# Kernel tuning notes

Measured on AMD Instinct MI355X. Metric: run time of the kernel, lower is better.

The kernel has to match this reference:

```python
import jax, jax.numpy as jnp
import numpy as np

N, E, B, O = 100000, 1600000, 256, 32
D, H, OD = 128, 128, 32  # node_features, hidden_dim, order_encoding_dim
L = 3  # num_layers


def setup_inputs() -> dict:
    key = jax.random.key(0)
    ks = jax.random.split(key, 32)
    g = lambda k, s, fan: jax.random.normal(k, s, jnp.float32) * (1.0 / np.sqrt(fan))
    inp = {
        'x': jax.random.normal(ks[0], (N, D), jnp.float32),
        'edge_index': jax.random.randint(ks[1], (2, E), 0, N),
        'orders': jax.random.normal(ks[2], (B, O, OD), jnp.float32),
        'batch': jnp.sort(jax.random.randint(ks[3], (N,), 0, B)),
        # GIN layers (input_dim == hidden_dim so all 3 layers stack): MLP = Lin(H,H)->ReLU->Lin(H,H), then BatchNorm1d
        'gW1': g(ks[4], (L, H, H), H), 'gb1': jnp.zeros((L, H)),
        'gW2': g(ks[5], (L, H, H), H), 'gb2': jnp.zeros((L, H)),
        'gamma': jnp.ones((L, H)), 'beta': jnp.zeros((L, H)),
        # order encoder: Lin(OD,H)->ReLU->Lin(H,H)
        'oW1': g(ks[6], (OD, H), OD), 'ob1': jnp.zeros((H,)),
        'oW2': g(ks[7], (H, H), H), 'ob2': jnp.zeros((H,)),
        # score head: Lin(4H,H)->ReLU->Lin(H,H//2)->ReLU->Lin(H//2,1)
        'sW1': g(ks[8], (4 * H, H), 4 * H), 'sb1': jnp.zeros((H,)),
        'sW2': g(ks[9], (H, H // 2), H), 'sb2': jnp.zeros((H // 2,)),
        'sW3': g(ks[10], (H // 2, 1), H // 2), 'sb3': jnp.zeros((1,)),
    }
    return inp


def reference(x, edge_index, orders, batch, gW1, gb1, gW2, gb2, gamma, beta,
              oW1, ob1, oW2, ob2, sW1, sb1, sW2, sb2, sW3, sb3):
    n = x.shape[0]
    src, dst = edge_index[0], edge_index[1]
    h = x
    nl = gW1.shape[0]
    for i in range(nl):  # fixed small layer count
        agg = jax.ops.segment_sum(h[src], dst, num_segments=n)  # sum aggregation
        z = agg + h  # (1 + eps) * x with eps = 0 (GINConv default)
        z = jnp.maximum(z @ gW1[i] + gb1[i], 0) @ gW2[i] + gb2[i]
        mu = z.mean(0)
        var = z.var(0)  # biased var, as torch BN uses for normalization
        z = (z - mu) * jax.lax.rsqrt(var + 1e-5) * gamma[i] + beta[i]
        h = jnp.maximum(z, 0) if i < nl - 1 else z  # dropout inactive (eval)
    b = orders.shape[0]
    cnt = jax.ops.segment_sum(jnp.ones((n,), h.dtype), batch, num_segments=b)
    ssum = jax.ops.segment_sum(h, batch, num_segments=b)
    smean = ssum / jnp.maximum(cnt, 1)[:, None]
    smax = jax.ops.segment_max(h, batch, num_segments=b)
    smax = jnp.where(jnp.isfinite(smax), smax, 0)
    graph = jnp.concatenate([smean, smax, ssum], axis=-1)  # [B, 3H]
    # batched over num_orders (equivalent to the python per-order loop)
    oe = jnp.maximum(orders @ oW1 + ob1, 0) @ oW2 + ob2  # [B, O, H]
    comb = jnp.concatenate(
        [jnp.broadcast_to(graph[:, None, :], (b, orders.shape[1], graph.shape[-1])), oe], axis=-1)
    s = jnp.maximum(comb @ sW1 + sb1, 0)
    s = jnp.maximum(s @ sW2 + sb2, 0)
    s = (s @ sW3 + sb3)[..., 0]  # [B, O]
    return s
```

## Files before the change

kernel.cpp:

```cpp
#include <hip/hip_runtime.h>

static constexpr int NN = 100000;
static constexpr int NE = 1600000;
static constexpr int NB = 256;
static constexpr int NO = 32;
static constexpr int HD = 128;
static constexpr long NH = (long)NN * HD;

static constexpr int BSHIFT = 9;
static constexpr int BSIZE = 1 << BSHIFT;
static constexpr int NBUCK = 256;
static constexpr int BCAP = 10240;
static constexpr int CHUNK = 16384;
static constexpr int NCHUNK = (NE + CHUNK - 1) / CHUNK;
static constexpr int POOL_ROWS = 64;
static constexpr int POOL_GRID = (NN + POOL_ROWS - 1) / POOL_ROWS;
static constexpr int NSUB = 64;
static constexpr int GATHER_GRID = NN / 4;

typedef _Float16 f16x8 __attribute__((ext_vector_type(8)));
typedef _Float16 f16x4 __attribute__((ext_vector_type(4)));
typedef _Float16 f16x2 __attribute__((ext_vector_type(2)));
typedef float f32x4 __attribute__((ext_vector_type(4)));

__device__ __forceinline__ unsigned int encf(float f) {
  unsigned int u = __float_as_uint(f);
  return (u & 0x80000000u) ? ~u : (u | 0x80000000u);
}
__device__ __forceinline__ float decf(unsigned int e) {
  return (e & 0x80000000u) ? __uint_as_float(e & 0x7fffffffu) : __uint_as_float(~e);
}

__global__ void bucket_scatter(const int* __restrict__ ei, int* __restrict__ cursor,
                               unsigned int* __restrict__ binned) {
  __shared__ int cnt[NBUCK];
  __shared__ int runbase[NBUCK];
  const int t = threadIdx.x;
  cnt[t] = 0;
  __syncthreads();
  long start = (long)blockIdx.x * CHUNK;
  long end = min((long)NE, start + CHUNK);
  for (long e = start + t; e < end; e += 256)
    atomicAdd(&cnt[ei[NE + e] >> BSHIFT], 1);
  __syncthreads();
  int c = cnt[t];
  runbase[t] = c ? atomicAdd(&cursor[t], c) : 0;
  cnt[t] = 0;
  __syncthreads();
  for (long e = start + t; e < end; e += 256) {
    int d = ei[NE + e], s = ei[e];
    int b = d >> BSHIFT;
    int pos = b * BCAP + runbase[b] + atomicAdd(&cnt[b], 1);
    binned[pos] = ((unsigned int)s << BSHIFT) | (unsigned int)(d & (BSIZE - 1));
  }
}

__global__ void bucket_csr(const unsigned int* __restrict__ binned,
                           const int* __restrict__ cursor,
                           int* __restrict__ rowStart, int* __restrict__ rowEnd,
                           int* __restrict__ col) {
  __shared__ int cnt[BSIZE];
  __shared__ int excl[BSIZE];
  __shared__ int cur[BSIZE];
  __shared__ int part[256];
  const int b = blockIdx.x;
  const int t = threadIdx.x;
  const int lo = b * BCAP;
  const int hi = lo + cursor[b];
  cnt[t] = 0; cnt[t + 256] = 0;
  __syncthreads();
  for (int i = lo + t; i < hi; i += 256)
    atomicAdd(&cnt[binned[i] & (BSIZE - 1)], 1);
  __syncthreads();
  int a0 = cnt[2 * t], a1 = cnt[2 * t + 1];
  int s = a0 + a1;
  part[t] = s;
  __syncthreads();
  for (int off = 1; off < 256; off <<= 1) {
    int u = (t >= off) ? part[t - off] : 0;
    __syncthreads();
    part[t] += u;
    __syncthreads();
  }
  int ebase = part[t] - s;
  excl[2 * t] = ebase;
  excl[2 * t + 1] = ebase + a0;
  __syncthreads();
  const int node0 = b * BSIZE;
  for (int i = t; i < BSIZE; i += 256) {
    int node = node0 + i;
    if (node < NN) {
      rowStart[node] = lo + excl[i];
      rowEnd[node]   = lo + excl[i] + cnt[i];
    }
    cur[i] = lo + excl[i];
  }
  __syncthreads();
  for (int i = lo + t; i < hi; i += 256) {
    unsigned int v = binned[i];
    int pos = atomicAdd(&cur[v & (BSIZE - 1)], 1);
    col[pos] = (int)(v >> BSHIFT);
  }
}

__global__ void f32to16_kernel(const float* __restrict__ in, _Float16* __restrict__ out) {
  long i = (long)(blockIdx.x * 256 + threadIdx.x) * 8;
  if (i >= NH) return;
  float4 a = *reinterpret_cast<const float4*>(in + i);
  float4 b = *reinterpret_cast<const float4*>(in + i + 4);
  f16x8 v;
  v[0] = (_Float16)a.x; v[1] = (_Float16)a.y; v[2] = (_Float16)a.z; v[3] = (_Float16)a.w;
  v[4] = (_Float16)b.x; v[5] = (_Float16)b.y; v[6] = (_Float16)b.z; v[7] = (_Float16)b.w;
  *reinterpret_cast<f16x8*>(out + i) = v;
}

__global__ void pack_w_kernel(const float* __restrict__ gW1, const float* __restrict__ gW2,
                              _Float16* __restrict__ Wp) {
  int tid = blockIdx.x * blockDim.x + threadIdx.x;
  if (tid >= 12288) return;
  int lane = tid & 63;
  int s = (tid >> 6) & 3;
  int t = (tid >> 8) & 7;
  int which = (tid >> 11) & 1;
  int layer = tid >> 12;
  const float* W = (which ? gW2 : gW1) + (long)layer * 128 * 128;
  _Float16* dst = Wp + (long)tid * 8;
  int kbase = s * 32 + ((lane >> 4) << 3);
  int n = t * 16 + (lane & 15);
#pragma unroll
  for (int j = 0; j < 8; ++j) dst[j] = (_Float16)W[(kbase + j) * 128 + n];
}

__global__ void pack_head_kernel(const float* __restrict__ oW1, const float* __restrict__ oW2,
                                 const float* __restrict__ sW1, const float* __restrict__ sW2,
                                 _Float16* __restrict__ dst) {
  int tid = blockIdx.x * blockDim.x + threadIdx.x;
  if (tid >= 5632) return;
  const float* W; int K, N, rowOff;
  int base = tid;
  if (tid < 512)       { W = oW1; K = 32;  N = 128; rowOff = 0;   }
  else if (tid < 2560) { W = oW2; K = 128; N = 128; rowOff = 0;   base = tid - 512; }
  else if (tid < 4608) { W = sW1; K = 128; N = 128; rowOff = 384; base = tid - 2560; }
  else                 { W = sW2; K = 128; N = 64;  rowOff = 0;   base = tid - 4608; }
  int lane = base & 63;
  int fs = base >> 6;
  int NS = K >> 5;
  int s = fs % NS;
  int tt = fs / NS;
  int k = s * 32 + ((lane >> 4) << 3);
  int n = tt * 16 + (lane & 15);
  _Float16* d = dst + (long)tid * 8;
#pragma unroll
  for (int j = 0; j < 8; ++j) d[j] = (_Float16)W[(long)(rowOff + k + j) * N + n];
}

__global__ void gather_kernel(const _Float16* __restrict__ hin, const int* __restrict__ rowStart,
                              const int* __restrict__ rowEnd, const int* __restrict__ col,
                              _Float16* __restrict__ z) {
  const int node = (blockIdx.x * blockDim.x + threadIdx.x) >> 6;
  if (node >= NN) return;
  const int c2 = (threadIdx.x & 63) * 2;
  auto ldh = [&](int n) -> float2 {
    f16x2 h = *reinterpret_cast<const f16x2*>(hin + (long)n * HD + c2);
    return make_float2((float)h[0], (float)h[1]);
  };
  const int lo = rowStart[node];
  const int hi = rowEnd[node];
  float2 acc = ldh(node);
  int j = lo;
  for (; j + 4 <= hi; j += 4) {
    int s0 = col[j], s1 = col[j + 1], s2 = col[j + 2], s3 = col[j + 3];
    float2 v0 = ldh(s0), v1 = ldh(s1), v2 = ldh(s2), v3 = ldh(s3);
    acc.x += (v0.x + v1.x) + (v2.x + v3.x);
    acc.y += (v0.y + v1.y) + (v2.y + v3.y);
  }
  if (j < hi) {
    int last = hi - 1;
    int s0 = col[j];
    int s1 = col[min(j + 1, last)];
    int s2 = col[min(j + 2, last)];
    int s3 = col[min(j + 3, last)];
    float m1 = (j + 1 < hi) ? 1.f : 0.f;
    float m2 = (j + 2 < hi) ? 1.f : 0.f;
    float m3 = (j + 3 < hi) ? 1.f : 0.f;
    float2 v0 = ldh(s0), v1 = ldh(s1), v2 = ldh(s2), v3 = ldh(s3);
    acc.x += v0.x + m1 * v1.x + m2 * v2.x + m3 * v3.x;
    acc.y += v0.y + m1 * v1.y + m2 * v2.y + m3 * v3.y;
  }
  f16x2 o;
  o[0] = (_Float16)acc.x;
  o[1] = (_Float16)acc.y;
  *reinterpret_cast<f16x2*>(z + (long)node * HD + c2) = o;
}

__global__ void __launch_bounds__(256)
fused_layer(const _Float16* __restrict__ Z, const _Float16* __restrict__ Wp,
            const float* __restrict__ b1, const float* __restrict__ b2,
            _Float16* __restrict__ Z2, float* __restrict__ accum2) {
  __shared__ _Float16 Abuf[64 * 136];
  __shared__ float red[256];
  const int t = threadIdx.x;
  const int row0 = blockIdx.x * 64;
  const int lane = t & 63;
  const int w = t >> 6;
  const int l15 = lane & 15;
  const int kgrp = lane >> 4;

  for (int idx = t; idx < 64 * 16; idx += 256) {
    int r = idx >> 4;
    int c8 = (idx & 15) * 8;
    int row = row0 + r;
    f16x8 v = {};
    if (row < NN) v = *reinterpret_cast<const f16x8*>(Z + (long)row * HD + c8);
    *reinterpret_cast<f16x8*>(&Abuf[r * 136 + c8]) = v;
  }
  red[t] = 0.f;
  __syncthreads();

  f32x4 acc[8];
  {
    f16x8 af[4];
#pragma unroll
    for (int s = 0; s < 4; ++s)
      af[s] = *reinterpret_cast<const f16x8*>(&Abuf[(w * 16 + l15) * 136 + s * 32 + kgrp * 8]);
    const _Float16* W1p = Wp;
#pragma unroll
    for (int tt = 0; tt < 8; ++tt) {
      float bb = b1[tt * 16 + l15];
      acc[tt] = (f32x4){bb, bb, bb, bb};
#pragma unroll
      for (int s = 0; s < 4; ++s) {
        f16x8 bf = *reinterpret_cast<const f16x8*>(W1p + ((tt * 4 + s) * 64 + lane) * 8);
        acc[tt] = __builtin_amdgcn_mfma_f32_16x16x32_f16(af[s], bf, acc[tt], 0, 0, 0);
      }
    }
  }
#pragma unroll
  for (int tt = 0; tt < 8; ++tt) {
#pragma unroll
    for (int j = 0; j < 4; ++j) {
      float v = fmaxf(acc[tt][j], 0.f);
      Abuf[(w * 16 + kgrp * 4 + j) * 136 + tt * 16 + l15] = (_Float16)v;
    }
  }
  {
    f16x8 af[4];
#pragma unroll
    for (int s = 0; s < 4; ++s)
      af[s] = *reinterpret_cast<const f16x8*>(&Abuf[(w * 16 + l15) * 136 + s * 32 + kgrp * 8]);
    const _Float16* W2p = Wp + 16384;
#pragma unroll
    for (int tt = 0; tt < 8; ++tt) {
      float bb = b2[tt * 16 + l15];
      acc[tt] = (f32x4){bb, bb, bb, bb};
#pragma unroll
      for (int s = 0; s < 4; ++s) {
        f16x8 bf = *reinterpret_cast<const f16x8*>(W2p + ((tt * 4 + s) * 64 + lane) * 8);
        acc[tt] = __builtin_amdgcn_mfma_f32_16x16x32_f16(af[s], bf, acc[tt], 0, 0, 0);
      }
    }
  }
#pragma unroll
  for (int tt = 0; tt < 8; ++tt) {
    int c = tt * 16 + l15;
    float s = 0.f, q = 0.f;
#pragma unroll
    for (int j = 0; j < 4; ++j) {
      int r = row0 + w * 16 + kgrp * 4 + j;
      if (r < NN) {
        float v = acc[tt][j];
        Z2[(long)r * HD + c] = (_Float16)v;
        s += v; q += v * v;
      }
    }
    atomicAdd(&red[c], s);
    atomicAdd(&red[128 + c], q);
  }
  __syncthreads();
  atomicAdd(&accum2[(blockIdx.x & (NSUB - 1)) * 256 + t], red[t]);
}

__global__ void bn_reduce(const float* __restrict__ accum2, const float* __restrict__ gamma,
                          const float* __restrict__ beta, float* __restrict__ scsh) {
  const int c = threadIdx.x;
  float s = 0.f;
  for (int i = 0; i < NSUB; ++i) s += accum2[i * 256 + c];
  __shared__ float red[256];
  red[c] = s;
  __syncthreads();
  if (c < 128) {
    const float n = (float)NN;
    float mu = red[c] / n;
    float var = red[128 + c] / n - mu * mu;
    float sc = rsqrtf(var + 1e-5f) * gamma[c];
    scsh[c] = sc;
    scsh[128 + c] = beta[c] - mu * sc;
  }
}

__global__ void bn_apply(const _Float16* __restrict__ z2, const float* __restrict__ scsh,
                         _Float16* __restrict__ hn) {
  long idx = (long)blockIdx.x * 256 + threadIdx.x;
  if (idx >= (long)NN * 16) return;
  int c8 = ((int)idx & 15) * 8;
  float4 sc0 = *reinterpret_cast<const float4*>(scsh + c8);
  float4 sc1 = *reinterpret_cast<const float4*>(scsh + c8 + 4);
  float4 sh0 = *reinterpret_cast<const float4*>(scsh + 128 + c8);
  float4 sh1 = *reinterpret_cast<const float4*>(scsh + 128 + c8 + 4);
  f16x8 v = *reinterpret_cast<const f16x8*>(z2 + idx * 8);
  f16x8 o;
  o[0] = (_Float16)fmaxf(fmaf((float)v[0], sc0.x, sh0.x), 0.f);
  o[1] = (_Float16)fmaxf(fmaf((float)v[1], sc0.y, sh0.y), 0.f);
  o[2] = (_Float16)fmaxf(fmaf((float)v[2], sc0.z, sh0.z), 0.f);
  o[3] = (_Float16)fmaxf(fmaf((float)v[3], sc0.w, sh0.w), 0.f);
  o[4] = (_Float16)fmaxf(fmaf((float)v[4], sc1.x, sh1.x), 0.f);
  o[5] = (_Float16)fmaxf(fmaf((float)v[5], sc1.y, sh1.y), 0.f);
  o[6] = (_Float16)fmaxf(fmaf((float)v[6], sc1.z, sh1.z), 0.f);
  o[7] = (_Float16)fmaxf(fmaf((float)v[7], sc1.w, sh1.w), 0.f);
  *reinterpret_cast<f16x8*>(hn + idx * 8) = o;
}

__global__ void pool_init(float* __restrict__ ssum, unsigned int* __restrict__ smaxU) {
  int i = blockIdx.x * 256 + threadIdx.x;
  ssum[i] = 0.f;
  smaxU[i] = 0x007FFFFFu;
}

__global__ void pool_partial(const _Float16* __restrict__ z2, const float* __restrict__ scsh,
                             const int* __restrict__ batch,
                             float* __restrict__ ssum, unsigned int* __restrict__ smaxU) {
  const int c = threadIdx.x;
  const int row0 = blockIdx.x * POOL_ROWS;
  const int rowEnd = min(row0 + POOL_ROWS, NN);
  const float sc = scsh[c];
  const float sh = scsh[128 + c];

  int curb = batch[row0];
  float s = 0.f, m = -INFINITY;
  for (int row = row0; row < rowEnd; ++row) {
    int b = batch[row];
    if (b != curb) {
      atomicAdd(&ssum[curb * HD + c], s);
      atomicMax(&smaxU[curb * HD + c], encf(m));
      s = 0.f; m = -INFINITY; curb = b;
    }
    float v = fmaf((float)z2[(long)row * HD + c], sc, sh);
    s += v;
    m = fmaxf(m, v);
  }
  atomicAdd(&ssum[curb * HD + c], s);
  atomicMax(&smaxU[curb * HD + c], encf(m));
}

__global__ void pool_final(const int* __restrict__ batch, float* __restrict__ ssum,
                           unsigned int* __restrict__ smaxU, float* __restrict__ smean,
                           float* __restrict__ smax) {
  const int b = blockIdx.x;
  const int c = threadIdx.x;
  int lo = 0, hi = NN;
  while (lo < hi) { int mid = (lo + hi) >> 1; if (batch[mid] < b) lo = mid + 1; else hi = mid; }
  const int start = lo;
  hi = NN;
  while (lo < hi) { int mid = (lo + hi) >> 1; if (batch[mid] < b + 1) lo = mid + 1; else hi = mid; }
  const int cnt = lo - start;
  float s = ssum[b * HD + c];
  smean[b * HD + c] = s / fmaxf((float)cnt, 1.f);
  smax[b * HD + c] = (cnt > 0) ? decf(smaxU[b * HD + c]) : 0.f;
}

__global__ void gpart_kernel(const float* __restrict__ smean, const float* __restrict__ smax,
                             const float* __restrict__ ssum, const float* __restrict__ sW1,
                             const float* __restrict__ sb1, float* __restrict__ gpart) {
  const int b = blockIdx.x;
  const int j = threadIdx.x;
  float acc = sb1[j];
  for (int k = 0; k < 128; ++k) acc = fmaf(smean[b * HD + k], sW1[k * 128 + j], acc);
  for (int k = 0; k < 128; ++k) acc = fmaf(smax[b * HD + k], sW1[(128 + k) * 128 + j], acc);
  for (int k = 0; k < 128; ++k) acc = fmaf(ssum[b * HD + k], sW1[(256 + k) * 128 + j], acc);
  gpart[b * HD + j] = acc;
}

__global__ void __launch_bounds__(128)
head_mfma(const float* __restrict__ orders, const _Float16* __restrict__ Wh,
          const float* __restrict__ ob1, const float* __restrict__ ob2,
          const float* __restrict__ gpart, const float* __restrict__ sb2,
          const float* __restrict__ sW3, const float* __restrict__ sb3,
          float* __restrict__ out) {
  __shared__ _Float16 B1[32 * 136];
  __shared__ _Float16 B2[32 * 136];
  const int t = threadIdx.x;
  const int g = blockIdx.x;
  const int row0 = g * 32;
  const int lane = t & 63;
  const int w = t >> 6;
  const int l15 = lane & 15;
  const int kgrp = lane >> 4;
  const _Float16* oW1p  = Wh;
  const _Float16* oW2p  = Wh + 4096;
  const _Float16* sW1bp = Wh + 20480;
  const _Float16* sW2p  = Wh + 36864;

  for (int idx = t; idx < 32 * 8; idx += 128) {
    int r = idx >> 3;
    int c4 = (idx & 7) * 4;
    float4 v = *reinterpret_cast<const float4*>(orders + (long)(row0 + r) * 32 + c4);
    f16x4 h;
    h[0] = (_Float16)v.x; h[1] = (_Float16)v.y; h[2] = (_Float16)v.z; h[3] = (_Float16)v.w;
    *reinterpret_cast<f16x4*>(&B1[r * 136 + c4]) = h;
  }
  __syncthreads();

  f32x4 acc[8];
  {
    f16x8 a0 = *reinterpret_cast<const f16x8*>(&B1[(w * 16 + l15) * 136 + kgrp * 8]);
#pragma unroll
    for (int tt = 0; tt < 8; ++tt) {
      float bb = ob1[tt * 16 + l15];
      acc[tt] = (f32x4){bb, bb, bb, bb};
      f16x8 bf = *reinterpret_cast<const f16x8*>(oW1p + (tt * 64 + lane) * 8);
      acc[tt] = __builtin_amdgcn_mfma_f32_16x16x32_f16(a0, bf, acc[tt], 0, 0, 0);
    }
#pragma unroll
    for (int tt = 0; tt < 8; ++tt)
#pragma unroll
      for (int j = 0; j < 4; ++j)
        B2[(w * 16 + kgrp * 4 + j) * 136 + tt * 16 + l15] = (_Float16)fmaxf(acc[tt][j], 0.f);
  }
  {
    f16x8 af[4];
#pragma unroll
    for (int s = 0; s < 4; ++s)
      af[s] = *reinterpret_cast<const f16x8*>(&B2[(w * 16 + l15) * 136 + s * 32 + kgrp * 8]);
#pragma unroll
    for (int tt = 0; tt < 8; ++tt) {
      float bb = ob2[tt * 16 + l15];
      acc[tt] = (f32x4){bb, bb, bb, bb};
#pragma unroll
      for (int s = 0; s < 4; ++s) {
        f16x8 bf = *reinterpret_cast<const f16x8*>(oW2p + ((tt * 4 + s) * 64 + lane) * 8);
        acc[tt] = __builtin_amdgcn_mfma_f32_16x16x32_f16(af[s], bf, acc[tt], 0, 0, 0);
      }
    }
#pragma unroll
    for (int tt = 0; tt < 8; ++tt)
#pragma unroll
      for (int j = 0; j < 4; ++j)
        B1[(w * 16 + kgrp * 4 + j) * 136 + tt * 16 + l15] = (_Float16)acc[tt][j];
  }
  {
    f16x8 af[4];
#pragma unroll
    for (int s = 0; s < 4; ++s)
      af[s] = *reinterpret_cast<const f16x8*>(&B1[(w * 16 + l15) * 136 + s * 32 + kgrp * 8]);
#pragma unroll
    for (int tt = 0; tt < 8; ++tt) {
      acc[tt] = (f32x4){0.f, 0.f, 0.f, 0.f};
#pragma unroll
      for (int s = 0; s < 4; ++s) {
        f16x8 bf = *reinterpret_cast<const f16x8*>(sW1bp + ((tt * 4 + s) * 64 + lane) * 8);
        acc[tt] = __builtin_amdgcn_mfma_f32_16x16x32_f16(af[s], bf, acc[tt], 0, 0, 0);
      }
    }
#pragma unroll
    for (int tt = 0; tt < 8; ++tt) {
      int c = tt * 16 + l15;
      float gp = gpart[g * HD + c];
#pragma unroll
      for (int j = 0; j < 4; ++j)
        B2[(w * 16 + kgrp * 4 + j) * 136 + c] = (_Float16)fmaxf(acc[tt][j] + gp, 0.f);
    }
  }
  {
    f16x8 af[4];
#pragma unroll
    for (int s = 0; s < 4; ++s)
      af[s] = *reinterpret_cast<const f16x8*>(&B2[(w * 16 + l15) * 136 + s * 32 + kgrp * 8]);
#pragma unroll
    for (int tt = 0; tt < 4; ++tt) {
      float bb = sb2[tt * 16 + l15];
      acc[tt] = (f32x4){bb, bb, bb, bb};
#pragma unroll
      for (int s = 0; s < 4; ++s) {
        f16x8 bf = *reinterpret_cast<const f16x8*>(sW2p + ((tt * 4 + s) * 64 + lane) * 8);
        acc[tt] = __builtin_amdgcn_mfma_f32_16x16x32_f16(af[s], bf, acc[tt], 0, 0, 0);
      }
    }
    float rsum[4] = {0.f, 0.f, 0.f, 0.f};
#pragma unroll
    for (int tt = 0; tt < 4; ++tt) {
      float wv = sW3[tt * 16 + l15];
#pragma unroll
      for (int j = 0; j < 4; ++j)
        rsum[j] = fmaf(fmaxf(acc[tt][j], 0.f), wv, rsum[j]);
    }
#pragma unroll
    for (int j = 0; j < 4; ++j) {
      rsum[j] += __shfl_xor(rsum[j], 1);
      rsum[j] += __shfl_xor(rsum[j], 2);
      rsum[j] += __shfl_xor(rsum[j], 4);
      rsum[j] += __shfl_xor(rsum[j], 8);
    }
    if (l15 == 0) {
      float b3 = sb3[0];
#pragma unroll
      for (int j = 0; j < 4; ++j)
        out[row0 + w * 16 + kgrp * 4 + j] = rsum[j] + b3;
    }
  }
}

extern "C" void kernel_launch(void* const* d_in, const int* in_sizes, int n_in,
                              void* d_out, int out_size, void* d_ws, size_t ws_size,
                              hipStream_t stream) {
  const float* x      = (const float*)d_in[0];
  const int*   ei     = (const int*)d_in[1];
  const float* orders = (const float*)d_in[2];
  const int*   batch  = (const int*)d_in[3];
  const float* gW1    = (const float*)d_in[4];
  const float* gb1    = (const float*)d_in[5];
  const float* gW2    = (const float*)d_in[6];
  const float* gb2    = (const float*)d_in[7];
  const float* gamma  = (const float*)d_in[8];
  const float* beta   = (const float*)d_in[9];
  const float* oW1    = (const float*)d_in[10];
  const float* ob1    = (const float*)d_in[11];
  const float* oW2    = (const float*)d_in[12];
  const float* ob2    = (const float*)d_in[13];
  const float* sW1    = (const float*)d_in[14];
  const float* sb1    = (const float*)d_in[15];
  const float* sW2    = (const float*)d_in[16];
  const float* sb2    = (const float*)d_in[17];
  const float* sW3    = (const float*)d_in[18];
  const float* sb3    = (const float*)d_in[19];
  float* out = (float*)d_out;

  char* ws = (char*)d_ws;
  _Float16* xh    = (_Float16*)ws;
  _Float16* bufAh = xh + NH;
  _Float16* bufCh = bufAh + NH;
  float* accum2 = (float*)(bufCh + NH);
  float* scsh   = accum2 + NSUB * 256;
  float* ssum   = scsh + 256;
  float* smean  = ssum + NB * HD;
  float* smax   = smean + NB * HD;
  unsigned int* smaxU = (unsigned int*)(smax + NB * HD);
  float* gpart = (float*)(smaxU + NB * HD);
  int* rowStart = (int*)(gpart + NB * HD);
  int* rowEnd   = rowStart + NN;
  int* col      = rowEnd + NN;
  unsigned int* binned = (unsigned int*)(col + NBUCK * BCAP);
  int* cursor = (int*)(binned + NBUCK * BCAP);
  _Float16* Wp  = (_Float16*)(cursor + NBUCK);
  _Float16* Wh  = Wp + 3 * 32768;

  hipMemsetAsync(cursor, 0, NBUCK * sizeof(int), stream);
  bucket_scatter<<<NCHUNK, 256, 0, stream>>>(ei, cursor, binned);
  bucket_csr<<<NBUCK, 256, 0, stream>>>(binned, cursor, rowStart, rowEnd, col);

  pack_w_kernel<<<48, 256, 0, stream>>>(gW1, gW2, Wp);
  pack_head_kernel<<<22, 256, 0, stream>>>(oW1, oW2, sW1, sW2, Wh);
  f32to16_kernel<<<(int)(NH / 8 + 255) / 256, 256, 0, stream>>>(x, xh);

  const int LAYER_GRID = (NN + 63) / 64;
  const int BA_GRID = (int)((NN * 16 + 255) / 256);
  for (int l = 0; l < 3; ++l) {
    gather_kernel<<<GATHER_GRID, 256, 0, stream>>>(xh, rowStart, rowEnd, col, bufAh);
    hipMemsetAsync(accum2, 0, NSUB * 256 * sizeof(float), stream);
    fused_layer<<<LAYER_GRID, 256, 0, stream>>>(
        bufAh, Wp + (long)l * 32768, gb1 + l * 128, gb2 + l * 128, bufCh, accum2);
    bn_reduce<<<1, 256, 0, stream>>>(accum2, gamma + l * 128, beta + l * 128, scsh);
    if (l < 2) bn_apply<<<BA_GRID, 256, 0, stream>>>(bufCh, scsh, xh);
  }

  pool_init<<<128, 256, 0, stream>>>(ssum, smaxU);
  pool_partial<<<POOL_GRID, 128, 0, stream>>>(bufCh, scsh, batch, ssum, smaxU);
  pool_final<<<NB, 128, 0, stream>>>(batch, ssum, smaxU, smean, smax);

  gpart_kernel<<<NB, 128, 0, stream>>>(smean, smax, ssum, sW1, sb1, gpart);
  head_mfma<<<NB, 128, 0, stream>>>(orders, Wh, ob1, ob2, gpart, sb2, sW3, sb3, out);
}
```

Baseline: 550.3 us.

## Enlarge GIN layer tiles, fuse pool_final with gpart, drop per-layer memsets

The fused GIN layer kernel now uses 512-thread blocks over 128-row tiles, so W fragments are loaded once per block for twice as many rows and the grid is halved. bn_reduce zeroes the BN accumulators after reading them, replacing the per-layer memset with a single one before the loop. pool_final and gpart_kernel are merged into one kernel that keeps pooled statistics in shared memory, which removes a launch and the smean/smax buffers. The larger block doubles shared-memory use per block and the launch bound of 512 with 8 may constrain registers.

```diff
diff --git a/kernel.cpp b/kernel.cpp
--- a/kernel.cpp
+++ b/kernel.cpp
@@ -193,20 +193,20 @@
   *reinterpret_cast<f16x2*>(z + (long)node * HD + c2) = o;
 }
 
-__global__ void __launch_bounds__(256)
+__global__ void __launch_bounds__(512, 8)
 fused_layer(const _Float16* __restrict__ Z, const _Float16* __restrict__ Wp,
             const float* __restrict__ b1, const float* __restrict__ b2,
             _Float16* __restrict__ Z2, float* __restrict__ accum2) {
-  __shared__ _Float16 Abuf[64 * 136];
+  __shared__ _Float16 Abuf[128 * 136];
   __shared__ float red[256];
   const int t = threadIdx.x;
-  const int row0 = blockIdx.x * 64;
+  const int row0 = blockIdx.x * 128;
   const int lane = t & 63;
   const int w = t >> 6;
   const int l15 = lane & 15;
   const int kgrp = lane >> 4;
 
-  for (int idx = t; idx < 64 * 16; idx += 256) {
+  for (int idx = t; idx < 128 * 16; idx += 512) {
     int r = idx >> 4;
     int c8 = (idx & 15) * 8;
     int row = row0 + r;
@@ -214,7 +214,7 @@
     if (row < NN) v = *reinterpret_cast<const f16x8*>(Z + (long)row * HD + c8);
     *reinterpret_cast<f16x8*>(&Abuf[r * 136 + c8]) = v;
   }
-  red[t] = 0.f;
+  if (t < 256) red[t] = 0.f;
   __syncthreads();
 
   f32x4 acc[8];
@@ -277,14 +277,17 @@
     atomicAdd(&red[128 + c], q);
   }
   __syncthreads();
-  atomicAdd(&accum2[(blockIdx.x & (NSUB - 1)) * 256 + t], red[t]);
-}
-
-__global__ void bn_reduce(const float* __restrict__ accum2, const float* __restrict__ gamma,
+  if (t < 256) atomicAdd(&accum2[(blockIdx.x & (NSUB - 1)) * 256 + t], red[t]);
+}
+
+__global__ void bn_reduce(float* __restrict__ accum2, const float* __restrict__ gamma,
                           const float* __restrict__ beta, float* __restrict__ scsh) {
   const int c = threadIdx.x;
   float s = 0.f;
-  for (int i = 0; i < NSUB; ++i) s += accum2[i * 256 + c];
+  for (int i = 0; i < NSUB; ++i) {
+    s += accum2[i * 256 + c];
+    accum2[i * 256 + c] = 0.f;
+  }
   __shared__ float red[256];
   red[c] = s;
   __syncthreads();
@@ -352,9 +355,10 @@
   atomicMax(&smaxU[curb * HD + c], encf(m));
 }
 
-__global__ void pool_final(const int* __restrict__ batch, float* __restrict__ ssum,
-                           unsigned int* __restrict__ smaxU, float* __restrict__ smean,
-                           float* __restrict__ smax) {
+__global__ void pool_gpart(const int* __restrict__ batch, const float* __restrict__ ssum,
+                           const unsigned int* __restrict__ smaxU, const float* __restrict__ sW1,
+                           const float* __restrict__ sb1, float* __restrict__ gpart) {
+  __shared__ float sm[128], sx[128], ss[128];
   const int b = blockIdx.x;
   const int c = threadIdx.x;
   int lo = 0, hi = NN;
@@ -364,20 +368,15 @@
   while (lo < hi) { int mid = (lo + hi) >> 1; if (batch[mid] < b + 1) lo = mid + 1; else hi = mid; }
   const int cnt = lo - start;
   float s = ssum[b * HD + c];
-  smean[b * HD + c] = s / fmaxf((float)cnt, 1.f);
-  smax[b * HD + c] = (cnt > 0) ? decf(smaxU[b * HD + c]) : 0.f;
-}
-
-__global__ void gpart_kernel(const float* __restrict__ smean, const float* __restrict__ smax,
-                             const float* __restrict__ ssum, const float* __restrict__ sW1,
-                             const float* __restrict__ sb1, float* __restrict__ gpart) {
-  const int b = blockIdx.x;
-  const int j = threadIdx.x;
-  float acc = sb1[j];
-  for (int k = 0; k < 128; ++k) acc = fmaf(smean[b * HD + k], sW1[k * 128 + j], acc);
-  for (int k = 0; k < 128; ++k) acc = fmaf(smax[b * HD + k], sW1[(128 + k) * 128 + j], acc);
-  for (int k = 0; k < 128; ++k) acc = fmaf(ssum[b * HD + k], sW1[(256 + k) * 128 + j], acc);
-  gpart[b * HD + j] = acc;
+  sm[c] = s / fmaxf((float)cnt, 1.f);
+  sx[c] = (cnt > 0) ? decf(smaxU[b * HD + c]) : 0.f;
+  ss[c] = s;
+  __syncthreads();
+  float acc = sb1[c];
+  for (int k = 0; k < 128; ++k) acc = fmaf(sm[k], sW1[k * 128 + c], acc);
+  for (int k = 0; k < 128; ++k) acc = fmaf(sx[k], sW1[(128 + k) * 128 + c], acc);
+  for (int k = 0; k < 128; ++k) acc = fmaf(ss[k], sW1[(256 + k) * 128 + c], acc);
+  gpart[b * HD + c] = acc;
 }
 
 __global__ void __launch_bounds__(128)
@@ -541,9 +540,7 @@
   float* accum2 = (float*)(bufCh + NH);
   float* scsh   = accum2 + NSUB * 256;
   float* ssum   = scsh + 256;
-  float* smean  = ssum + NB * HD;
-  float* smax   = smean + NB * HD;
-  unsigned int* smaxU = (unsigned int*)(smax + NB * HD);
+  unsigned int* smaxU = (unsigned int*)(ssum + NB * HD);
   float* gpart = (float*)(smaxU + NB * HD);
   int* rowStart = (int*)(gpart + NB * HD);
   int* rowEnd   = rowStart + NN;
@@ -560,13 +557,13 @@
   pack_w_kernel<<<48, 256, 0, stream>>>(gW1, gW2, Wp);
   pack_head_kernel<<<22, 256, 0, stream>>>(oW1, oW2, sW1, sW2, Wh);
   f32to16_kernel<<<(int)(NH / 8 + 255) / 256, 256, 0, stream>>>(x, xh);
-
-  const int LAYER_GRID = (NN + 63) / 64;
+  hipMemsetAsync(accum2, 0, NSUB * 256 * sizeof(float), stream);
+
+  const int LAYER_GRID = (NN + 127) / 128;
   const int BA_GRID = (int)((NN * 16 + 255) / 256);
   for (int l = 0; l < 3; ++l) {
     gather_kernel<<<GATHER_GRID, 256, 0, stream>>>(xh, rowStart, rowEnd, col, bufAh);
-    hipMemsetAsync(accum2, 0, NSUB * 256 * sizeof(float), stream);
-    fused_layer<<<LAYER_GRID, 256, 0, stream>>>(
+    fused_layer<<<LAYER_GRID, 512, 0, stream>>>(
         bufAh, Wp + (long)l * 32768, gb1 + l * 128, gb2 + l * 128, bufCh, accum2);
     bn_reduce<<<1, 256, 0, stream>>>(accum2, gamma + l * 128, beta + l * 128, scsh);
     if (l < 2) bn_apply<<<BA_GRID, 256, 0, stream>>>(bufCh, scsh, xh);
@@ -574,8 +571,7 @@
 
   pool_init<<<128, 256, 0, stream>>>(ssum, smaxU);
   pool_partial<<<POOL_GRID, 128, 0, stream>>>(bufCh, scsh, batch, ssum, smaxU);
-  pool_final<<<NB, 128, 0, stream>>>(batch, ssum, smaxU, smean, smax);
-
-  gpart_kernel<<<NB, 128, 0, stream>>>(smean, smax, ssum, sW1, sb1, gpart);
+  pool_gpart<<<NB, 128, 0, stream>>>(batch, ssum, smaxU, sW1, sb1, gpart);
+
   head_mfma<<<NB, 128, 0, stream>>>(orders, Wh, ob1, ob2, gpart, sb2, sW3, sb3, out);
 }
```

After: 568.9 us. +3.4%, slower.
